# Kernel optimization log

Hardware: AMD Instinct MI355X
Metric: run time of the kernel (lower is better)

## Reference

```python
import jax, jax.numpy as jnp
import numpy as np

NUM_HEADS = 16
THETA = 10000.0
B, S, D = 2, 2048, 1024
D_K = D // NUM_HEADS


def setup_inputs() -> dict:
    key = jax.random.key(0)
    ks = jax.random.split(key, 5)
    s = 0.02
    return {
        "x": jax.random.normal(ks[0], (B, S, D), dtype=jnp.float32),
        "W_q": jax.random.normal(ks[1], (D, D), dtype=jnp.float32) * s,
        "W_k": jax.random.normal(ks[2], (D, D), dtype=jnp.float32) * s,
        "W_v": jax.random.normal(ks[3], (D, D), dtype=jnp.float32) * s,
        "W_o": jax.random.normal(ks[4], (D, D), dtype=jnp.float32) * s,
        "token_positions": jnp.arange(S, dtype=jnp.int32),
    }


def _rope(x, token_positions):
    # x: [..., seq, d_k]; equivalent to the block-diagonal 2x2 rotation matmul
    d2 = x.shape[-1] // 2
    inv_freq = THETA ** (-(2.0 * jnp.arange(d2, dtype=x.dtype)) / x.shape[-1])  # [d2]
    ang = token_positions.astype(x.dtype)[:, None] * inv_freq[None, :]  # [seq, d2]
    cos, sin = jnp.cos(ang), jnp.sin(ang)
    xp = x.reshape(x.shape[:-1] + (d2, 2))
    xe, xo = xp[..., 0], xp[..., 1]
    oe = cos * xe - sin * xo
    oo = sin * xe + cos * xo
    return jnp.stack([oe, oo], axis=-1).reshape(x.shape)


def reference(x, W_q, W_k, W_v, W_o, token_positions):
    seq = x.shape[-2]
    # QKV projections (weights stored as [out, in])
    Q = jnp.einsum('bsd,ed->bse', x, W_q)
    K = jnp.einsum('bsd,ed->bse', x, W_k)
    V = jnp.einsum('bsd,ed->bse', x, W_v)
    def split_heads(t):
        return t.reshape(t.shape[:-1] + (NUM_HEADS, D_K)).swapaxes(-3, -2)  # [b,h,s,dk]
    Q, K, V = split_heads(Q), split_heads(K), split_heads(V)
    Q = _rope(Q, token_positions)
    K = _rope(K, token_positions)
    scale = 1.0 / np.sqrt(D_K)
    scores = jnp.einsum('bhqd,bhkd->bhqk', Q, K) * scale
    causal = jnp.tril(jnp.ones((seq, seq), dtype=bool))
    scores = jnp.where(causal, scores, -jnp.inf)
    probs = jax.nn.softmax(scores, axis=-1)
    out = jnp.einsum('bhqk,bhkd->bhqd', probs, V)
    out = out.swapaxes(-3, -2).reshape(x.shape[:-1] + (D,))
    return jnp.einsum('bse,de->bsd', out, W_o)
```

## Files before the change

kernel.cpp:

```cpp
#include <hip/hip_runtime.h>
#include <hip/hip_bf16.h>
#include <math.h>

#define H_    16
#define DK_   64
#define Dm    1024
#define Bb    2
#define Ss    2048
#define Mrows 4096

typedef short s16x8 __attribute__((ext_vector_type(8)));
typedef float f32x4 __attribute__((ext_vector_type(4)));
typedef unsigned short u16;

__device__ __forceinline__ u16 f2b(float f) {
  __hip_bfloat16 h = __float2bfloat16(f);
  return *reinterpret_cast<u16*>(&h);
}
__device__ __forceinline__ float b2f(u16 u) {
  __hip_bfloat16 h;
  *reinterpret_cast<u16*>(&h) = u;
  return __bfloat162float(h);
}

#define GLDS(g, l)                                                             \
  __builtin_amdgcn_global_load_lds(                                            \
      (const __attribute__((address_space(1))) unsigned int*)(g),              \
      (__attribute__((address_space(3))) unsigned int*)(l), 16, 0, 0)

__device__ __forceinline__ int SW64(int row, int col) {
  return row * 64 + ((((col >> 3) ^ (row & 7) ^ (row >> 3)) & 7) << 3) + (col & 7);
}

__global__ __launch_bounds__(256) void k_cast(const float* __restrict__ s,
                                              u16* __restrict__ d, int n4) {
  int i = blockIdx.x * 256 + threadIdx.x;
  if (i >= n4) return;
  float4 v = reinterpret_cast<const float4*>(s)[i];
  ushort4 o;
  o.x = f2b(v.x); o.y = f2b(v.y); o.z = f2b(v.z); o.w = f2b(v.w);
  reinterpret_cast<ushort4*>(d)[i] = o;
}

__global__ __launch_bounds__(256) void k_cast4(const float* __restrict__ s0, const float* __restrict__ s1,
                                               const float* __restrict__ s2, const float* __restrict__ s3,
                                               u16* __restrict__ d0, u16* __restrict__ d1,
                                               u16* __restrict__ d2, u16* __restrict__ d3) {
  int y = blockIdx.y;
  const float* s = (y == 0) ? s0 : (y == 1) ? s1 : (y == 2) ? s2 : s3;
  u16* d = (y == 0) ? d0 : (y == 1) ? d1 : (y == 2) ? d2 : d3;
  int i = blockIdx.x * 256 + threadIdx.x;
  float4 v = reinterpret_cast<const float4*>(s)[i];
  ushort4 o;
  o.x = f2b(v.x); o.y = f2b(v.y); o.z = f2b(v.z); o.w = f2b(v.w);
  reinterpret_cast<ushort4*>(d)[i] = o;
}

__global__ __launch_bounds__(256) void k_rope(u16* __restrict__ Q, u16* __restrict__ K,
                                              const int* __restrict__ pos) {
  int idx = blockIdx.x * 256 + threadIdx.x;
  if (idx >= Mrows * (Dm / 2)) return;
  int row = idx >> 9;
  int pc  = idx & 511;
  int i   = pc & 31;
  int h   = pc >> 5;
  int col = h * 64 + i * 2;
  float p   = (float)pos[row & (Ss - 1)];
  float inv = powf(10000.0f, -(float)i / 32.0f);
  float ang = p * inv;
  float sn = sinf(ang), cs = cosf(ang);
  size_t o = (size_t)row * Dm + col;
  {
    float xe = b2f(Q[o]), xo = b2f(Q[o + 1]);
    Q[o]     = f2b(cs * xe - sn * xo);
    Q[o + 1] = f2b(sn * xe + cs * xo);
  }
  {
    float xe = b2f(K[o]), xo = b2f(K[o + 1]);
    K[o]     = f2b(cs * xe - sn * xo);
    K[o + 1] = f2b(sn * xe + cs * xo);
  }
}

template <int BN>
__global__ __launch_bounds__(256) void k_gemm_bt(
    const u16* __restrict__ A,
    const u16* __restrict__ B0, const u16* __restrict__ B1, const u16* __restrict__ B2,
    u16* __restrict__ O0, u16* __restrict__ O1, u16* __restrict__ OVT,
    float* __restrict__ OF, int M, int N, int K, int f32out) {
  constexpr int NFR = BN / 32;
  __shared__ __align__(16) u16 lsA[128 * 32];
  __shared__ __align__(16) u16 lsB[BN * 32];
  const int tid = threadIdx.x, lane = tid & 63, wave = tid >> 6;
  const int quad = lane >> 4, l16 = lane & 15;
  const int wrow = wave >> 1, wcol = wave & 1;
  const int m0 = blockIdx.x * 128, n0 = blockIdx.y * BN;
  const int z = blockIdx.z;
  const u16* Bp = (z == 0) ? B0 : (z == 1) ? B1 : B2;
  u16* Op = (z == 0) ? O0 : O1;
  f32x4 acc[4][NFR] = {};

  for (int k0 = 0; k0 < K; k0 += 32) {
#pragma unroll
    for (int c = 0; c < 2; ++c) {
      int f = (wave * 2 + c) * 512 + lane * 8;
      int row = f >> 5, colk = f & 31;
      GLDS(A + (size_t)(m0 + row) * K + k0 + colk, lsA + (wave * 2 + c) * 512);
    }
#pragma unroll
    for (int c = 0; c < BN / 64; ++c) {
      int cc = wave * (BN / 64) + c;
      int f = cc * 512 + lane * 8;
      int row = f >> 5, colk = f & 31;
      GLDS(Bp + (size_t)(n0 + row) * K + k0 + colk, lsB + cc * 512);
    }
    __syncthreads();
    s16x8 af[4], bfr[NFR];
#pragma unroll
    for (int i = 0; i < 4; ++i)
      af[i] = *reinterpret_cast<const s16x8*>(&lsA[(wrow * 64 + i * 16 + l16) * 32 + quad * 8]);
#pragma unroll
    for (int i = 0; i < NFR; ++i)
      bfr[i] = *reinterpret_cast<const s16x8*>(&lsB[(wcol * (BN / 2) + i * 16 + l16) * 32 + quad * 8]);
#pragma unroll
    for (int mi = 0; mi < 4; ++mi)
#pragma unroll
      for (int ni = 0; ni < NFR; ++ni)
        acc[mi][ni] = __builtin_amdgcn_mfma_f32_16x16x32_bf16(af[mi], bfr[ni], acc[mi][ni], 0, 0, 0);
    __syncthreads();
  }

  if (!f32out && z == 2) {
#pragma unroll
    for (int mi = 0; mi < 4; ++mi)
#pragma unroll
      for (int ni = 0; ni < NFR; ++ni) {
        int row0 = m0 + wrow * 64 + mi * 16 + quad * 4;
        int col  = n0 + wcol * (BN / 2) + ni * 16 + l16;
        int bb = row0 >> 11, s0 = row0 & (Ss - 1);
        ushort4 pk;
        pk.x = f2b(acc[mi][ni][0]); pk.y = f2b(acc[mi][ni][1]);
        pk.z = f2b(acc[mi][ni][2]); pk.w = f2b(acc[mi][ni][3]);
        *reinterpret_cast<ushort4*>(&OVT[((size_t)bb * Dm + col) * Ss + s0]) = pk;
      }
    return;
  }
#pragma unroll
  for (int mi = 0; mi < 4; ++mi)
#pragma unroll
    for (int ni = 0; ni < NFR; ++ni)
#pragma unroll
      for (int r = 0; r < 4; ++r) {
        int row = m0 + wrow * 64 + mi * 16 + quad * 4 + r;
        int col = n0 + wcol * (BN / 2) + ni * 16 + l16;
        float v = acc[mi][ni][r];
        size_t idx = (size_t)row * N + col;
        if (f32out) OF[idx] = v;
        else        Op[idx] = f2b(v);
      }
}

__global__ __launch_bounds__(256) void k_flash(const u16* __restrict__ Q,
                                               const u16* __restrict__ K,
                                               const u16* __restrict__ VT,
                                               u16* __restrict__ O) {
  __shared__ __align__(16) u16 lsK[64 * 64];
  __shared__ __align__(16) u16 lsVT[64 * 64];
  __shared__ __align__(16) u16 lsP[4][16 * 64];
  const int tid = threadIdx.x, lane = tid & 63, wave = tid >> 6;
  const int quad = lane >> 4, l16 = lane & 15;
  const int bid = blockIdx.x;
  const int bh = bid & 31;
  const int h = bh & (H_ - 1), b = bh >> 4;
  const int q0 = (bid >> 5) * 64;
  const int qrow = q0 + wave * 16;
  const int xorv = (l16 * 2) & 0xE;

  const size_t qoff = (size_t)(b * Ss + qrow + l16) * Dm + h * 64;
  s16x8 qf0 = *reinterpret_cast<const s16x8*>(&Q[qoff + quad * 8]);
  s16x8 qf1 = *reinterpret_cast<const s16x8*>(&Q[qoff + 32 + quad * 8]);
#pragma unroll
  for (int j = 0; j < 8; ++j) {
    qf0[j] = (short)f2b(b2f((u16)qf0[j]) * 0.125f);
    qf1[j] = (short)f2b(b2f((u16)qf1[j]) * 0.125f);
  }

  f32x4 ot[4] = {};
  float m_i = -INFINITY, l_i = 0.f;
  const int ktmax = q0 >> 6;
  const int c0 = wave * 2;

  for (int kt = 0; kt <= ktmax; ++kt) {
    const size_t kbase  = (size_t)(b * Ss + kt * 64) * Dm + h * 64;
    const size_t vtbase = ((size_t)b * Dm + h * 64) * Ss + kt * 64;
#pragma unroll
    for (int c = 0; c < 2; ++c) {
      int slot = (c0 + c) * 64 + lane;
      int row = slot >> 3;
      int g = ((slot & 7) ^ (row & 7) ^ (row >> 3)) & 7;
      GLDS(K  + kbase  + (size_t)row * Dm + g * 8, lsK  + (c0 + c) * 512);
      GLDS(VT + vtbase + (size_t)row * Ss + g * 8, lsVT + (c0 + c) * 512);
    }
    __syncthreads();

    f32x4 st[4] = {};
#pragma unroll
    for (int kc = 0; kc < 2; ++kc) {
      s16x8 qf = kc ? qf1 : qf0;
#pragma unroll
      for (int ni = 0; ni < 4; ++ni) {
        s16x8 kf = *reinterpret_cast<const s16x8*>(&lsK[SW64(ni * 16 + l16, kc * 32 + quad * 8)]);
        st[ni] = __builtin_amdgcn_mfma_f32_16x16x32_bf16(kf, qf, st[ni], 0, 0, 0);
      }
    }
    if (kt == ktmax) {
      int gq = qrow + l16;
#pragma unroll
      for (int ni = 0; ni < 4; ++ni)
#pragma unroll
        for (int r = 0; r < 4; ++r)
          if (kt * 64 + ni * 16 + quad * 4 + r > gq) st[ni][r] = -INFINITY;
    }

    float mx = -INFINITY;
#pragma unroll
    for (int ni = 0; ni < 4; ++ni)
#pragma unroll
      for (int r = 0; r < 4; ++r) mx = fmaxf(mx, st[ni][r]);
    mx = fmaxf(mx, __shfl_xor(mx, 16));
    mx = fmaxf(mx, __shfl_xor(mx, 32));
    float mnew = fmaxf(m_i, mx);
    float alpha = __expf(m_i - mnew);
    m_i = mnew;
    float rs = 0.f;
#pragma unroll
    for (int ni = 0; ni < 4; ++ni)
#pragma unroll
      for (int r = 0; r < 4; ++r) {
        float p = __expf(st[ni][r] - mnew);
        st[ni][r] = p;
        rs += p;
      }
    rs += __shfl_xor(rs, 16);
    rs += __shfl_xor(rs, 32);
    l_i = l_i * alpha + rs;
#pragma unroll
    for (int ni = 0; ni < 4; ++ni) ot[ni] *= alpha;

#pragma unroll
    for (int ni = 0; ni < 4; ++ni) {
      ushort4 pk;
      pk.x = f2b(st[ni][0]); pk.y = f2b(st[ni][1]);
      pk.z = f2b(st[ni][2]); pk.w = f2b(st[ni][3]);
      *reinterpret_cast<ushort4*>(&lsP[wave][l16 * 64 + (((ni * 4 + quad) ^ xorv) << 2)]) = pk;
    }
#pragma unroll
    for (int kc = 0; kc < 2; ++kc) {
      s16x8 pf = *reinterpret_cast<const s16x8*>(
          &lsP[wave][l16 * 64 + ((((kc * 8 + quad * 2)) ^ xorv) << 2)]);
#pragma unroll
      for (int ni = 0; ni < 4; ++ni) {
        s16x8 vf = *reinterpret_cast<const s16x8*>(&lsVT[SW64(ni * 16 + l16, kc * 32 + quad * 8)]);
        ot[ni] = __builtin_amdgcn_mfma_f32_16x16x32_bf16(vf, pf, ot[ni], 0, 0, 0);
      }
    }
    __syncthreads();
  }

  float inv = 1.0f / l_i;
  const size_t obase = (size_t)(b * Ss + qrow + l16) * Dm + h * 64;
#pragma unroll
  for (int ni = 0; ni < 4; ++ni) {
    ushort4 pk;
    pk.x = f2b(ot[ni][0] * inv); pk.y = f2b(ot[ni][1] * inv);
    pk.z = f2b(ot[ni][2] * inv); pk.w = f2b(ot[ni][3] * inv);
    *reinterpret_cast<ushort4*>(&O[obase + ni * 16 + quad * 4]) = pk;
  }
}

extern "C" void kernel_launch(void* const* d_in, const int* in_sizes, int n_in,
                              void* d_out, int out_size, void* d_ws, size_t ws_size,
                              hipStream_t stream) {
  const float* x  = (const float*)d_in[0];
  const float* Wq = (const float*)d_in[1];
  const float* Wk = (const float*)d_in[2];
  const float* Wv = (const float*)d_in[3];
  const float* Wo = (const float*)d_in[4];
  const int* pos  = (const int*)d_in[5];
  float* out = (float*)d_out;

  char* w = (char*)d_ws;
  u16* xb  = (u16*)w; w += (size_t)Mrows * Dm * 2;
  u16* wqb = (u16*)w; w += (size_t)Dm * Dm * 2;
  u16* wkb = (u16*)w; w += (size_t)Dm * Dm * 2;
  u16* wvb = (u16*)w; w += (size_t)Dm * Dm * 2;
  u16* wob = (u16*)w; w += (size_t)Dm * Dm * 2;
  u16* Qb  = (u16*)w; w += (size_t)Mrows * Dm * 2;
  u16* Kb  = (u16*)w; w += (size_t)Mrows * Dm * 2;
  u16* VTb = (u16*)w; w += (size_t)Mrows * Dm * 2;
  u16* Ab  = (u16*)w; w += (size_t)Mrows * Dm * 2;

  k_cast<<<Mrows * Dm / 1024, 256, 0, stream>>>(x, xb, Mrows * Dm / 4);
  k_cast4<<<dim3(Dm * Dm / 1024, 4), 256, 0, stream>>>(Wq, Wk, Wv, Wo, wqb, wkb, wvb, wob);

  k_gemm_bt<128><<<dim3(32, 8, 3), 256, 0, stream>>>(xb, wqb, wkb, wvb,
                                                     Qb, Kb, VTb, nullptr,
                                                     Mrows, Dm, Dm, 0);
  k_rope<<<(Mrows * 512) / 256, 256, 0, stream>>>(Qb, Kb, pos);
  k_flash<<<dim3(1024), 256, 0, stream>>>(Qb, Kb, VTb, Ab);
  k_gemm_bt<64><<<dim3(32, 16, 1), 256, 0, stream>>>(Ab, wob, wob, wob,
                                                     nullptr, nullptr, nullptr, out,
                                                     Mrows, Dm, Dm, 1);
}
```

Before: 214.8 us.

## Fuse RoPE and softmax scale into QKV GEMM epilogue, widen flash tiles

Drops the separate RoPE kernel. A small cos/sin table is precomputed and the rotation, plus the Q scale folded with log2(e), is applied in the QKV GEMM epilogue using lane shuffles. The flash kernel now handles 128 query rows per block, 32 per wave, reusing each K/V tile for two MFMA row groups. It pairs light and heavy causal tiles across the grid, switches to exp2, and removes the per-load Q rescale. This saves a full read-modify-write pass over Q and K and halves K/V tile loads, at the cost of more registers and a doubled P buffer in LDS.

Result: slower. 232.4 us (+8.2%).

```diff
diff --git a/kernel.cpp b/kernel.cpp
--- a/kernel.cpp
+++ b/kernel.cpp
@@ -8,6 +8,7 @@
 #define Bb    2
 #define Ss    2048
 #define Mrows 4096
+#define QSCALE 0.1803368801f
 
 typedef short s16x8 __attribute__((ext_vector_type(8)));
 typedef float f32x4 __attribute__((ext_vector_type(4)));
@@ -56,30 +57,13 @@
   reinterpret_cast<ushort4*>(d)[i] = o;
 }
 
-__global__ __launch_bounds__(256) void k_rope(u16* __restrict__ Q, u16* __restrict__ K,
-                                              const int* __restrict__ pos) {
-  int idx = blockIdx.x * 256 + threadIdx.x;
-  if (idx >= Mrows * (Dm / 2)) return;
-  int row = idx >> 9;
-  int pc  = idx & 511;
-  int i   = pc & 31;
-  int h   = pc >> 5;
-  int col = h * 64 + i * 2;
-  float p   = (float)pos[row & (Ss - 1)];
-  float inv = powf(10000.0f, -(float)i / 32.0f);
-  float ang = p * inv;
-  float sn = sinf(ang), cs = cosf(ang);
-  size_t o = (size_t)row * Dm + col;
-  {
-    float xe = b2f(Q[o]), xo = b2f(Q[o + 1]);
-    Q[o]     = f2b(cs * xe - sn * xo);
-    Q[o + 1] = f2b(sn * xe + cs * xo);
-  }
-  {
-    float xe = b2f(K[o]), xo = b2f(K[o + 1]);
-    K[o]     = f2b(cs * xe - sn * xo);
-    K[o + 1] = f2b(sn * xe + cs * xo);
-  }
+__global__ __launch_bounds__(256) void k_ropetab(const int* __restrict__ pos,
+                                                 float2* __restrict__ tab) {
+  int t = blockIdx.x * 256 + threadIdx.x;
+  int s = t >> 5, i = t & 31;
+  float p = (float)pos[s];
+  float ang = p * powf(10000.0f, -(float)i / 32.0f);
+  tab[t] = make_float2(cosf(ang), sinf(ang));
 }
 
 template <int BN>
@@ -87,7 +71,8 @@
     const u16* __restrict__ A,
     const u16* __restrict__ B0, const u16* __restrict__ B1, const u16* __restrict__ B2,
     u16* __restrict__ O0, u16* __restrict__ O1, u16* __restrict__ OVT,
-    float* __restrict__ OF, int M, int N, int K, int f32out) {
+    float* __restrict__ OF, const float2* __restrict__ tab,
+    int M, int N, int K, int f32out) {
   constexpr int NFR = BN / 32;
   __shared__ __align__(16) u16 lsA[128 * 32];
   __shared__ __align__(16) u16 lsB[BN * 32];
@@ -145,6 +130,27 @@
       }
     return;
   }
+
+  if (tab && z < 2) {
+    float qs = (z == 0) ? QSCALE : 1.0f;
+#pragma unroll
+    for (int mi = 0; mi < 4; ++mi)
+#pragma unroll
+      for (int ni = 0; ni < NFR; ++ni) {
+        int col = n0 + wcol * (BN / 2) + ni * 16 + l16;
+        int ip = (col >> 1) & 31;
+        float sgn = (col & 1) ? 1.0f : -1.0f;
+#pragma unroll
+        for (int r = 0; r < 4; ++r) {
+          int row = (m0 + wrow * 64 + mi * 16 + quad * 4 + r) & (Ss - 1);
+          float2 cs = tab[row * 32 + ip];
+          float v = acc[mi][ni][r] * qs;
+          float p = __shfl_xor(v, 1);
+          acc[mi][ni][r] = cs.x * v + cs.y * sgn * p;
+        }
+      }
+  }
+
 #pragma unroll
   for (int mi = 0; mi < 4; ++mi)
 #pragma unroll
@@ -166,115 +172,130 @@
                                                u16* __restrict__ O) {
   __shared__ __align__(16) u16 lsK[64 * 64];
   __shared__ __align__(16) u16 lsVT[64 * 64];
-  __shared__ __align__(16) u16 lsP[4][16 * 64];
+  __shared__ __align__(16) u16 lsP[4][32 * 64];
   const int tid = threadIdx.x, lane = tid & 63, wave = tid >> 6;
   const int quad = lane >> 4, l16 = lane & 15;
   const int bid = blockIdx.x;
   const int bh = bid & 31;
   const int h = bh & (H_ - 1), b = bh >> 4;
-  const int q0 = (bid >> 5) * 64;
-  const int qrow = q0 + wave * 16;
+  const int g = bid >> 5, a = g & 7, bsel = g >> 3;
+  const int qt = bsel ? (15 - a) : a;
+  const int q0 = qt * 128;
+  const int qbase = q0 + wave * 32;
+  const int ktmax_w = (qbase + 31) >> 6;
+  const int ktmax_b = (q0 + 127) >> 6;
   const int xorv = (l16 * 2) & 0xE;
 
-  const size_t qoff = (size_t)(b * Ss + qrow + l16) * Dm + h * 64;
-  s16x8 qf0 = *reinterpret_cast<const s16x8*>(&Q[qoff + quad * 8]);
-  s16x8 qf1 = *reinterpret_cast<const s16x8*>(&Q[qoff + 32 + quad * 8]);
-#pragma unroll
-  for (int j = 0; j < 8; ++j) {
-    qf0[j] = (short)f2b(b2f((u16)qf0[j]) * 0.125f);
-    qf1[j] = (short)f2b(b2f((u16)qf1[j]) * 0.125f);
-  }
-
-  f32x4 ot[4] = {};
-  float m_i = -INFINITY, l_i = 0.f;
-  const int ktmax = q0 >> 6;
+  s16x8 qf[2][2];
+#pragma unroll
+  for (int s = 0; s < 2; ++s) {
+    const size_t qoff = (size_t)(b * Ss + qbase + s * 16 + l16) * Dm + h * 64;
+    qf[s][0] = *reinterpret_cast<const s16x8*>(&Q[qoff + quad * 8]);
+    qf[s][1] = *reinterpret_cast<const s16x8*>(&Q[qoff + 32 + quad * 8]);
+  }
+
+  f32x4 ot[2][4] = {};
+  float m_i[2] = {-INFINITY, -INFINITY}, l_i[2] = {0.f, 0.f};
   const int c0 = wave * 2;
 
-  for (int kt = 0; kt <= ktmax; ++kt) {
+  for (int kt = 0; kt <= ktmax_b; ++kt) {
     const size_t kbase  = (size_t)(b * Ss + kt * 64) * Dm + h * 64;
     const size_t vtbase = ((size_t)b * Dm + h * 64) * Ss + kt * 64;
 #pragma unroll
     for (int c = 0; c < 2; ++c) {
       int slot = (c0 + c) * 64 + lane;
       int row = slot >> 3;
-      int g = ((slot & 7) ^ (row & 7) ^ (row >> 3)) & 7;
-      GLDS(K  + kbase  + (size_t)row * Dm + g * 8, lsK  + (c0 + c) * 512);
-      GLDS(VT + vtbase + (size_t)row * Ss + g * 8, lsVT + (c0 + c) * 512);
+      int gg = ((slot & 7) ^ (row & 7) ^ (row >> 3)) & 7;
+      GLDS(K  + kbase  + (size_t)row * Dm + gg * 8, lsK  + (c0 + c) * 512);
+      GLDS(VT + vtbase + (size_t)row * Ss + gg * 8, lsVT + (c0 + c) * 512);
     }
     __syncthreads();
 
-    f32x4 st[4] = {};
-#pragma unroll
-    for (int kc = 0; kc < 2; ++kc) {
-      s16x8 qf = kc ? qf1 : qf0;
-#pragma unroll
-      for (int ni = 0; ni < 4; ++ni) {
-        s16x8 kf = *reinterpret_cast<const s16x8*>(&lsK[SW64(ni * 16 + l16, kc * 32 + quad * 8)]);
-        st[ni] = __builtin_amdgcn_mfma_f32_16x16x32_bf16(kf, qf, st[ni], 0, 0, 0);
-      }
-    }
-    if (kt == ktmax) {
-      int gq = qrow + l16;
-#pragma unroll
-      for (int ni = 0; ni < 4; ++ni)
-#pragma unroll
-        for (int r = 0; r < 4; ++r)
-          if (kt * 64 + ni * 16 + quad * 4 + r > gq) st[ni][r] = -INFINITY;
-    }
-
-    float mx = -INFINITY;
-#pragma unroll
-    for (int ni = 0; ni < 4; ++ni)
-#pragma unroll
-      for (int r = 0; r < 4; ++r) mx = fmaxf(mx, st[ni][r]);
-    mx = fmaxf(mx, __shfl_xor(mx, 16));
-    mx = fmaxf(mx, __shfl_xor(mx, 32));
-    float mnew = fmaxf(m_i, mx);
-    float alpha = __expf(m_i - mnew);
-    m_i = mnew;
-    float rs = 0.f;
-#pragma unroll
-    for (int ni = 0; ni < 4; ++ni)
-#pragma unroll
-      for (int r = 0; r < 4; ++r) {
-        float p = __expf(st[ni][r] - mnew);
-        st[ni][r] = p;
-        rs += p;
-      }
-    rs += __shfl_xor(rs, 16);
-    rs += __shfl_xor(rs, 32);
-    l_i = l_i * alpha + rs;
-#pragma unroll
-    for (int ni = 0; ni < 4; ++ni) ot[ni] *= alpha;
-
+    if (kt <= ktmax_w) {
+      f32x4 st[2][4] = {};
+#pragma unroll
+      for (int kc = 0; kc < 2; ++kc)
+#pragma unroll
+        for (int ni = 0; ni < 4; ++ni) {
+          s16x8 kf = *reinterpret_cast<const s16x8*>(&lsK[SW64(ni * 16 + l16, kc * 32 + quad * 8)]);
+          st[0][ni] = __builtin_amdgcn_mfma_f32_16x16x32_bf16(kf, qf[0][kc], st[0][ni], 0, 0, 0);
+          st[1][ni] = __builtin_amdgcn_mfma_f32_16x16x32_bf16(kf, qf[1][kc], st[1][ni], 0, 0, 0);
+        }
+      if (kt == ktmax_w) {
+#pragma unroll
+        for (int s = 0; s < 2; ++s) {
+          int gq = qbase + s * 16 + l16;
+#pragma unroll
+          for (int ni = 0; ni < 4; ++ni)
+#pragma unroll
+            for (int r = 0; r < 4; ++r)
+              if (kt * 64 + ni * 16 + quad * 4 + r > gq) st[s][ni][r] = -INFINITY;
+        }
+      }
+
+#pragma unroll
+      for (int s = 0; s < 2; ++s) {
+        float mx = -INFINITY;
+#pragma unroll
+        for (int ni = 0; ni < 4; ++ni)
+#pragma unroll
+          for (int r = 0; r < 4; ++r) mx = fmaxf(mx, st[s][ni][r]);
+        mx = fmaxf(mx, __shfl_xor(mx, 16));
+        mx = fmaxf(mx, __shfl_xor(mx, 32));
+        float mnew = fmaxf(m_i[s], mx);
+        float alpha = exp2f(m_i[s] - mnew);
+        m_i[s] = mnew;
+        float rs = 0.f;
+#pragma unroll
+        for (int ni = 0; ni < 4; ++ni)
+#pragma unroll
+          for (int r = 0; r < 4; ++r) {
+            float p = exp2f(st[s][ni][r] - mnew);
+            st[s][ni][r] = p;
+            rs += p;
+          }
+        rs += __shfl_xor(rs, 16);
+        rs += __shfl_xor(rs, 32);
+        l_i[s] = l_i[s] * alpha + rs;
+#pragma unroll
+        for (int ni = 0; ni < 4; ++ni) ot[s][ni] *= alpha;
+#pragma unroll
+        for (int ni = 0; ni < 4; ++ni) {
+          ushort4 pk;
+          pk.x = f2b(st[s][ni][0]); pk.y = f2b(st[s][ni][1]);
+          pk.z = f2b(st[s][ni][2]); pk.w = f2b(st[s][ni][3]);
+          *reinterpret_cast<ushort4*>(
+              &lsP[wave][(s * 16 + l16) * 64 + (((ni * 4 + quad) ^ xorv) << 2)]) = pk;
+        }
+      }
+#pragma unroll
+      for (int kc = 0; kc < 2; ++kc) {
+        s16x8 pf0 = *reinterpret_cast<const s16x8*>(
+            &lsP[wave][l16 * 64 + (((kc * 8 + quad * 2) ^ xorv) << 2)]);
+        s16x8 pf1 = *reinterpret_cast<const s16x8*>(
+            &lsP[wave][(16 + l16) * 64 + (((kc * 8 + quad * 2) ^ xorv) << 2)]);
+#pragma unroll
+        for (int ni = 0; ni < 4; ++ni) {
+          s16x8 vf = *reinterpret_cast<const s16x8*>(&lsVT[SW64(ni * 16 + l16, kc * 32 + quad * 8)]);
+          ot[0][ni] = __builtin_amdgcn_mfma_f32_16x16x32_bf16(vf, pf0, ot[0][ni], 0, 0, 0);
+          ot[1][ni] = __builtin_amdgcn_mfma_f32_16x16x32_bf16(vf, pf1, ot[1][ni], 0, 0, 0);
+        }
+      }
+    }
+    __syncthreads();
+  }
+
+#pragma unroll
+  for (int s = 0; s < 2; ++s) {
+    float inv = 1.0f / l_i[s];
+    const size_t obase = (size_t)(b * Ss + qbase + s * 16 + l16) * Dm + h * 64;
 #pragma unroll
     for (int ni = 0; ni < 4; ++ni) {
       ushort4 pk;
-      pk.x = f2b(st[ni][0]); pk.y = f2b(st[ni][1]);
-      pk.z = f2b(st[ni][2]); pk.w = f2b(st[ni][3]);
-      *reinterpret_cast<ushort4*>(&lsP[wave][l16 * 64 + (((ni * 4 + quad) ^ xorv) << 2)]) = pk;
-    }
-#pragma unroll
-    for (int kc = 0; kc < 2; ++kc) {
-      s16x8 pf = *reinterpret_cast<const s16x8*>(
-          &lsP[wave][l16 * 64 + ((((kc * 8 + quad * 2)) ^ xorv) << 2)]);
-#pragma unroll
-      for (int ni = 0; ni < 4; ++ni) {
-        s16x8 vf = *reinterpret_cast<const s16x8*>(&lsVT[SW64(ni * 16 + l16, kc * 32 + quad * 8)]);
-        ot[ni] = __builtin_amdgcn_mfma_f32_16x16x32_bf16(vf, pf, ot[ni], 0, 0, 0);
-      }
-    }
-    __syncthreads();
-  }
-
-  float inv = 1.0f / l_i;
-  const size_t obase = (size_t)(b * Ss + qrow + l16) * Dm + h * 64;
-#pragma unroll
-  for (int ni = 0; ni < 4; ++ni) {
-    ushort4 pk;
-    pk.x = f2b(ot[ni][0] * inv); pk.y = f2b(ot[ni][1] * inv);
-    pk.z = f2b(ot[ni][2] * inv); pk.w = f2b(ot[ni][3] * inv);
-    *reinterpret_cast<ushort4*>(&O[obase + ni * 16 + quad * 4]) = pk;
+      pk.x = f2b(ot[s][ni][0] * inv); pk.y = f2b(ot[s][ni][1] * inv);
+      pk.z = f2b(ot[s][ni][2] * inv); pk.w = f2b(ot[s][ni][3] * inv);
+      *reinterpret_cast<ushort4*>(&O[obase + ni * 16 + quad * 4]) = pk;
+    }
   }
 }
 
@@ -299,16 +320,17 @@
   u16* Kb  = (u16*)w; w += (size_t)Mrows * Dm * 2;
   u16* VTb = (u16*)w; w += (size_t)Mrows * Dm * 2;
   u16* Ab  = (u16*)w; w += (size_t)Mrows * Dm * 2;
+  float2* tabf = (float2*)w; w += (size_t)Ss * 32 * sizeof(float2);
 
   k_cast<<<Mrows * Dm / 1024, 256, 0, stream>>>(x, xb, Mrows * Dm / 4);
   k_cast4<<<dim3(Dm * Dm / 1024, 4), 256, 0, stream>>>(Wq, Wk, Wv, Wo, wqb, wkb, wvb, wob);
+  k_ropetab<<<Ss * 32 / 256, 256, 0, stream>>>(pos, tabf);
 
   k_gemm_bt<128><<<dim3(32, 8, 3), 256, 0, stream>>>(xb, wqb, wkb, wvb,
-                                                     Qb, Kb, VTb, nullptr,
+                                                     Qb, Kb, VTb, nullptr, tabf,
                                                      Mrows, Dm, Dm, 0);
-  k_rope<<<(Mrows * 512) / 256, 256, 0, stream>>>(Qb, Kb, pos);
-  k_flash<<<dim3(1024), 256, 0, stream>>>(Qb, Kb, VTb, Ab);
+  k_flash<<<dim3(512), 256, 0, stream>>>(Qb, Kb, VTb, Ab);
   k_gemm_bt<64><<<dim3(32, 16, 1), 256, 0, stream>>>(Ab, wob, wob, wob,
-                                                     nullptr, nullptr, nullptr, out,
+                                                     nullptr, nullptr, nullptr, out, nullptr,
                                                      Mrows, Dm, Dm, 1);
 }
```
